# Performance work log

Hardware: AMD Instinct MI355X
Metric: run time of the kernel (lower is better)

Reference implementation:

```python
import jax, jax.numpy as jnp
import numpy as np

N_USERS, N_ITEMS, D, E = 60000, 40000, 64, 1600000
N = N_USERS + N_ITEMS


def setup_inputs() -> dict:
    key = jax.random.key(0)
    ks = jax.random.split(key, 7)
    user_embedding = jax.random.normal(ks[0], (N_USERS, D), dtype=jnp.float32)
    item_embedding = jax.random.normal(ks[1], (N_ITEMS, D), dtype=jnp.float32)
    # per-node symmetric-normalization scalar (e.g. 1/sqrt(deg)), positive
    norm = jax.random.uniform(ks[2], (N, 1), dtype=jnp.float32, minval=0.01, maxval=1.0)
    src = jax.random.randint(ks[3], (E,), 0, N, dtype=jnp.int32)
    dst = jax.random.randint(ks[4], (E,), 0, N, dtype=jnp.int32)
    # xavier-uniform linear weights, stored as [out_dim, in_dim] like nn.Linear
    limit = float(np.sqrt(6.0 / (D + D)))
    W1 = jax.random.uniform(ks[5], (D, D), dtype=jnp.float32, minval=-limit, maxval=limit)
    W2 = jax.random.uniform(ks[6], (D, D), dtype=jnp.float32, minval=-limit, maxval=limit)
    return {"user_embedding": user_embedding, "item_embedding": item_embedding,
            "norm": norm, "src": src, "dst": dst, "W1": W1, "W2": W2}


def reference(user_embedding, item_embedding, norm, src, dst, W1, W2):
    h = jnp.concatenate([user_embedding, item_embedding], axis=0)  # [N, D]
    # W1(h) can be computed once per node, then gathered per edge.
    h1 = h @ W1.T                                                  # [N, D]
    hs = h[src]                                                    # [E, D] gather
    hd = h[dst]                                                    # [E, D] gather
    # message: W1(h_src) + W2(h_src * h_dst), scaled by norm_src * norm_dst
    msg = (h1[src] + (hs * hd) @ W2.T) * (norm[src] * norm[dst])   # [E, D]
    m = jax.ops.segment_sum(msg, dst, num_segments=h.shape[0])     # scatter-sum -> [N, D]
    m = m + h1
    out = jnp.where(m >= 0, m, 0.2 * m)  # LeakyReLU(0.2); dropout=0 (eval) is identity
    # F.normalize(p=2, dim=1), eps=1e-12
    l2 = jnp.sqrt(jnp.sum(out * out, axis=1, keepdims=True))
    return out / jnp.maximum(l2, 1e-12)
```

## Files before the change

kernel.cpp:

```cpp
#include <hip/hip_runtime.h>

#define DD 64

typedef __attribute__((ext_vector_type(8))) short bfrag;
typedef __attribute__((ext_vector_type(4))) float ffrag;

static __device__ __forceinline__ short f2bf(float f) {
  union { float f; unsigned u; } v; v.f = f;
  unsigned r = v.u + 0x7fff + ((v.u >> 16) & 1);
  return (short)(r >> 16);
}
static __device__ __forceinline__ float bf2f(unsigned short u) {
  union { unsigned u; float f; } v; v.u = ((unsigned)u) << 16; return v.f;
}


__global__ void chist_kernel(const int* __restrict__ dst, int* __restrict__ ccnt,
                             int E, int NB) {
  __shared__ int ch[512];
  for (int i = threadIdx.x; i < 512; i += 256) ch[i] = 0;
  __syncthreads();
  int ebase = blockIdx.x * 4096;
#pragma unroll
  for (int j = 0; j < 16; ++j) {
    int e = ebase + j * 256 + threadIdx.x;
    if (e < E) atomicAdd(&ch[dst[e] >> 8], 1);
  }
  __syncthreads();
  for (int b = threadIdx.x; b < NB; b += 256) {
    int c = ch[b];
    if (c) atomicAdd(&ccnt[b], c);
  }
}

__global__ void cscan_kernel(const int* __restrict__ ccnt, int* __restrict__ cbase,
                             int* __restrict__ ccursor, int NB) {
  __shared__ int wtot[4];
  int t = threadIdx.x;
  int i0 = t * 2, i1 = t * 2 + 1;
  int v0 = (i0 < NB) ? ccnt[i0] : 0;
  int v1 = (i1 < NB) ? ccnt[i1] : 0;
  int s = v0 + v1;
  int lane = t & 63, w = t >> 6;
  int ps = s;
#pragma unroll
  for (int off = 1; off < 64; off <<= 1) {
    int tmp = __shfl_up(ps, off);
    if (lane >= off) ps += tmp;
  }
  if (lane == 63) wtot[w] = ps;
  __syncthreads();
  int wbase = 0;
  for (int k = 0; k < w; ++k) wbase += wtot[k];
  int excl = wbase + ps - s;
  if (i0 < NB) { cbase[i0] = excl;      ccursor[i0] = excl; }
  if (i1 < NB) { cbase[i1] = excl + v0; ccursor[i1] = excl + v0; }
  if (t == 0) {
    int tot = 0;
    for (int k = 0; k < 4; ++k) tot += wtot[k];
    cbase[NB] = tot;
  }
}

__global__ void cscatter_kernel(const int* __restrict__ src, const int* __restrict__ dst,
                                int* __restrict__ ccursor, unsigned* __restrict__ pairb,
                                int E, int NB) {
  __shared__ int bh[512], bbase[512], brank[512];
  for (int i = threadIdx.x; i < 512; i += 256) { bh[i] = 0; brank[i] = 0; }
  __syncthreads();
  int ebase = blockIdx.x * 4096;
  int se[16], de[16];
#pragma unroll
  for (int j = 0; j < 16; ++j) {
    int e = ebase + j * 256 + threadIdx.x;
    if (e < E) {
      se[j] = src[e];
      de[j] = dst[e];
      atomicAdd(&bh[de[j] >> 8], 1);
    } else {
      se[j] = -1; de[j] = 0;
    }
  }
  __syncthreads();
  for (int b = threadIdx.x; b < NB; b += 256) {
    int c = bh[b];
    bbase[b] = c ? atomicAdd(&ccursor[b], c) : 0;
  }
  __syncthreads();
#pragma unroll
  for (int j = 0; j < 16; ++j) {
    if (se[j] >= 0) {
      int b = de[j] >> 8;
      int r = atomicAdd(&brank[b], 1);
      pairb[bbase[b] + r] = ((unsigned)se[j] << 8) | (unsigned)(de[j] & 255);
    }
  }
}

__global__ void fine_kernel(const unsigned* __restrict__ pairb,
                            const int* __restrict__ cbase,
                            int* __restrict__ offs, int* __restrict__ cnt,
                            int* __restrict__ ebuf, int Nn) {
  __shared__ int fh[256], fcur[256];
  __shared__ int wtot[4];
  int t = threadIdx.x, b = blockIdx.x;
  int nb0 = b << 8;
  int cbeg = cbase[b], cend = cbase[b + 1];
  fh[t] = 0;
  __syncthreads();
  for (int p = cbeg + t; p < cend; p += 256) atomicAdd(&fh[pairb[p] & 255u], 1);
  __syncthreads();
  int val = fh[t];
  int lane = t & 63, w = t >> 6;
  int ps = val;
#pragma unroll
  for (int off = 1; off < 64; off <<= 1) {
    int tmp = __shfl_up(ps, off);
    if (lane >= off) ps += tmp;
  }
  if (lane == 63) wtot[w] = ps;
  __syncthreads();
  int wbase = 0;
  for (int k = 0; k < w; ++k) wbase += wtot[k];
  int excl = wbase + ps - val;
  int node = nb0 + t;
  if (node < Nn) { offs[node] = cbeg + excl; cnt[node] = val; }
  fcur[t] = cbeg + excl;
  __syncthreads();
  for (int p = cbeg + t; p < cend; p += 256) {
    unsigned v = pairb[p];
    int pos = atomicAdd(&fcur[v & 255u], 1);
    ebuf[pos] = (int)(v >> 8);
  }
}


__global__ void hconv_kernel(const float* __restrict__ ue, const float* __restrict__ ie,
                             const float* __restrict__ norm,
                             unsigned short* __restrict__ hsc, int Nn, int NU) {
  int tid = blockIdx.x * blockDim.x + threadIdx.x;
  if (tid >= Nn * 16) return;
  int row = tid >> 4;
  int q = tid & 15;
  const float* hr = (row < NU) ? ue + (size_t)row * DD : ie + (size_t)(row - NU) * DD;
  float nr = norm[row];
  float4 hv = reinterpret_cast<const float4*>(hr)[q];
  unsigned u0 = (unsigned short)f2bf(nr * hv.x);
  unsigned u1 = (unsigned short)f2bf(nr * hv.y);
  unsigned u2 = (unsigned short)f2bf(nr * hv.z);
  unsigned u3 = (unsigned short)f2bf(nr * hv.w);
  uint2 pk;
  pk.x = u0 | (u1 << 16);
  pk.y = u2 | (u3 << 16);
  *reinterpret_cast<uint2*>(hsc + (size_t)row * DD + q * 4) = pk;
}

__launch_bounds__(256)
__global__ void gather8_kernel(const unsigned short* __restrict__ hsc,
                               const int* __restrict__ offs,
                               const int* __restrict__ cnt,
                               const int* __restrict__ ebuf,
                               unsigned short* __restrict__ g, int Nn) {
  int lane = threadIdx.x & 63;
  int wid = blockIdx.x * 4 + (threadIdx.x >> 6);
  int d = __builtin_amdgcn_readfirstlane(wid);
  if (d >= Nn) return;
  int beg = __builtin_amdgcn_readfirstlane(offs[d]);
  int num = __builtin_amdgcn_readfirstlane(cnt[d]);
  float a0 = 0.f, a1 = 0.f, a2 = 0.f, a3 = 0.f;
  float a4 = 0.f, a5 = 0.f, a6 = 0.f, a7 = 0.f;
  int i = 0;
  for (; i + 8 <= num; i += 8) {
    int s0 = ebuf[beg + i + 0];
    int s1 = ebuf[beg + i + 1];
    int s2 = ebuf[beg + i + 2];
    int s3 = ebuf[beg + i + 3];
    int s4 = ebuf[beg + i + 4];
    int s5 = ebuf[beg + i + 5];
    int s6 = ebuf[beg + i + 6];
    int s7 = ebuf[beg + i + 7];
    a0 += bf2f(hsc[(size_t)s0 * DD + lane]);
    a1 += bf2f(hsc[(size_t)s1 * DD + lane]);
    a2 += bf2f(hsc[(size_t)s2 * DD + lane]);
    a3 += bf2f(hsc[(size_t)s3 * DD + lane]);
    a4 += bf2f(hsc[(size_t)s4 * DD + lane]);
    a5 += bf2f(hsc[(size_t)s5 * DD + lane]);
    a6 += bf2f(hsc[(size_t)s6 * DD + lane]);
    a7 += bf2f(hsc[(size_t)s7 * DD + lane]);
  }
  for (; i + 4 <= num; i += 4) {
    int s0 = ebuf[beg + i + 0];
    int s1 = ebuf[beg + i + 1];
    int s2 = ebuf[beg + i + 2];
    int s3 = ebuf[beg + i + 3];
    a0 += bf2f(hsc[(size_t)s0 * DD + lane]);
    a1 += bf2f(hsc[(size_t)s1 * DD + lane]);
    a2 += bf2f(hsc[(size_t)s2 * DD + lane]);
    a3 += bf2f(hsc[(size_t)s3 * DD + lane]);
  }
  for (; i < num; ++i) a0 += bf2f(hsc[(size_t)ebuf[beg + i] * DD + lane]);
  float r = ((a0 + a1) + (a2 + a3)) + ((a4 + a5) + (a6 + a7));
  g[(size_t)d * DD + lane] = (unsigned short)f2bf(r);
}

__launch_bounds__(256)
__global__ void gather8f_kernel(const unsigned short* __restrict__ hsc,
                                const int* __restrict__ offs,
                                const int* __restrict__ cnt,
                                const int* __restrict__ ebuf,
                                float* __restrict__ g, int Nn) {
  int lane = threadIdx.x & 63;
  int wid = blockIdx.x * 4 + (threadIdx.x >> 6);
  int d = __builtin_amdgcn_readfirstlane(wid);
  if (d >= Nn) return;
  int beg = __builtin_amdgcn_readfirstlane(offs[d]);
  int num = __builtin_amdgcn_readfirstlane(cnt[d]);
  float a0 = 0.f, a1 = 0.f, a2 = 0.f, a3 = 0.f;
  float a4 = 0.f, a5 = 0.f, a6 = 0.f, a7 = 0.f;
  int i = 0;
  for (; i + 8 <= num; i += 8) {
    int s0 = ebuf[beg + i + 0];
    int s1 = ebuf[beg + i + 1];
    int s2 = ebuf[beg + i + 2];
    int s3 = ebuf[beg + i + 3];
    int s4 = ebuf[beg + i + 4];
    int s5 = ebuf[beg + i + 5];
    int s6 = ebuf[beg + i + 6];
    int s7 = ebuf[beg + i + 7];
    a0 += bf2f(hsc[(size_t)s0 * DD + lane]);
    a1 += bf2f(hsc[(size_t)s1 * DD + lane]);
    a2 += bf2f(hsc[(size_t)s2 * DD + lane]);
    a3 += bf2f(hsc[(size_t)s3 * DD + lane]);
    a4 += bf2f(hsc[(size_t)s4 * DD + lane]);
    a5 += bf2f(hsc[(size_t)s5 * DD + lane]);
    a6 += bf2f(hsc[(size_t)s6 * DD + lane]);
    a7 += bf2f(hsc[(size_t)s7 * DD + lane]);
  }
  for (; i + 4 <= num; i += 4) {
    int s0 = ebuf[beg + i + 0];
    int s1 = ebuf[beg + i + 1];
    int s2 = ebuf[beg + i + 2];
    int s3 = ebuf[beg + i + 3];
    a0 += bf2f(hsc[(size_t)s0 * DD + lane]);
    a1 += bf2f(hsc[(size_t)s1 * DD + lane]);
    a2 += bf2f(hsc[(size_t)s2 * DD + lane]);
    a3 += bf2f(hsc[(size_t)s3 * DD + lane]);
  }
  for (; i < num; ++i) a0 += bf2f(hsc[(size_t)ebuf[beg + i] * DD + lane]);
  g[(size_t)d * DD + lane] = ((a0 + a1) + (a2 + a3)) + ((a4 + a5) + (a6 + a7));
}

__launch_bounds__(256)
__global__ void node_hsc_kernel(const unsigned short* __restrict__ hsc,
                                const unsigned short* __restrict__ g,
                                const float* __restrict__ norm,
                                const float* __restrict__ W1,
                                const float* __restrict__ W2,
                                float* __restrict__ out, int Nn) {
  int lane = threadIdx.x & 63;
  int l15 = lane & 15;
  int lg  = lane >> 4;
  int tile = blockIdx.x * 4 + (threadIdx.x >> 6);

  bfrag w1f[2][4], w2f[2][4];
#pragma unroll
  for (int jt = 0; jt < 4; ++jt) {
    int wrow = jt * 16 + l15;
#pragma unroll
    for (int ks = 0; ks < 2; ++ks) {
      int kb = ks * 32 + lg * 8;
      const float* p1 = W1 + wrow * DD + kb;
      const float* p2 = W2 + wrow * DD + kb;
#pragma unroll
      for (int j = 0; j < 8; ++j) {
        w1f[ks][jt][j] = f2bf(p1[j]);
        w2f[ks][jt][j] = f2bf(p2[j]);
      }
    }
  }

  if (tile * 16 >= Nn) return;
  int node = tile * 16 + l15;
  int nc = (node < Nn) ? node : (Nn - 1);
  float nd = norm[nc];
  float rnd = 1.0f / nd;

  ffrag acc[4];
#pragma unroll
  for (int jt = 0; jt < 4; ++jt) acc[jt] = (ffrag){0.f, 0.f, 0.f, 0.f};

#pragma unroll
  for (int ks = 0; ks < 2; ++ks) {
    int kb = ks * 32 + lg * 8;
    bfrag gb = *reinterpret_cast<const bfrag*>(g + (size_t)nc * DD + kb);
    bfrag hb = *reinterpret_cast<const bfrag*>(hsc + (size_t)nc * DD + kb);
    bfrag xf, yf;
#pragma unroll
    for (int j = 0; j < 8; ++j) {
      float gv = bf2f((unsigned short)gb[j]);
      float hj = bf2f((unsigned short)hb[j]);
      xf[j] = f2bf(fmaf(nd, gv, hj * rnd));
      yf[j] = f2bf(gv * hj);
    }
#pragma unroll
    for (int jt = 0; jt < 4; ++jt) {
      acc[jt] = __builtin_amdgcn_mfma_f32_16x16x32_bf16(xf, w1f[ks][jt], acc[jt], 0, 0, 0);
      acc[jt] = __builtin_amdgcn_mfma_f32_16x16x32_bf16(yf, w2f[ks][jt], acc[jt], 0, 0, 0);
    }
  }

  float v[4][4];
  float ss[4];
#pragma unroll
  for (int r = 0; r < 4; ++r) {
    float s = 0.f;
#pragma unroll
    for (int jt = 0; jt < 4; ++jt) {
      float m = acc[jt][r];
      float t = (m >= 0.f) ? m : 0.2f * m;
      v[r][jt] = t;
      s = fmaf(t, t, s);
    }
#pragma unroll
    for (int off = 1; off < 16; off <<= 1) s += __shfl_xor(s, off);
    ss[r] = s;
  }
#pragma unroll
  for (int r = 0; r < 4; ++r) {
    int orow = tile * 16 + lg * 4 + r;
    if (orow < Nn) {
      float inv = 1.0f / fmaxf(sqrtf(ss[r]), 1e-12f);
#pragma unroll
      for (int jt = 0; jt < 4; ++jt)
        out[(size_t)orow * DD + jt * 16 + l15] = v[r][jt] * inv;
    }
  }
}

__launch_bounds__(256)
__global__ void node_hscf_kernel(const unsigned short* __restrict__ hsc,
                                 const float* __restrict__ g,
                                 const float* __restrict__ norm,
                                 const float* __restrict__ W1,
                                 const float* __restrict__ W2,
                                 float* __restrict__ out, int Nn) {
  int lane = threadIdx.x & 63;
  int l15 = lane & 15;
  int lg  = lane >> 4;
  int tile = blockIdx.x * 4 + (threadIdx.x >> 6);

  bfrag w1f[2][4], w2f[2][4];
#pragma unroll
  for (int jt = 0; jt < 4; ++jt) {
    int wrow = jt * 16 + l15;
#pragma unroll
    for (int ks = 0; ks < 2; ++ks) {
      int kb = ks * 32 + lg * 8;
      const float* p1 = W1 + wrow * DD + kb;
      const float* p2 = W2 + wrow * DD + kb;
#pragma unroll
      for (int j = 0; j < 8; ++j) {
        w1f[ks][jt][j] = f2bf(p1[j]);
        w2f[ks][jt][j] = f2bf(p2[j]);
      }
    }
  }

  if (tile * 16 >= Nn) return;
  int node = tile * 16 + l15;
  int nc = (node < Nn) ? node : (Nn - 1);
  float nd = norm[nc];
  float rnd = 1.0f / nd;

  ffrag acc[4];
#pragma unroll
  for (int jt = 0; jt < 4; ++jt) acc[jt] = (ffrag){0.f, 0.f, 0.f, 0.f};

#pragma unroll
  for (int ks = 0; ks < 2; ++ks) {
    int kb = ks * 32 + lg * 8;
    float4 g0 = *reinterpret_cast<const float4*>(g + (size_t)nc * DD + kb);
    float4 g1 = *reinterpret_cast<const float4*>(g + (size_t)nc * DD + kb + 4);
    bfrag hb = *reinterpret_cast<const bfrag*>(hsc + (size_t)nc * DD + kb);
    float gv[8] = {g0.x, g0.y, g0.z, g0.w, g1.x, g1.y, g1.z, g1.w};
    bfrag xf, yf;
#pragma unroll
    for (int j = 0; j < 8; ++j) {
      float hj = bf2f((unsigned short)hb[j]);
      xf[j] = f2bf(fmaf(nd, gv[j], hj * rnd));
      yf[j] = f2bf(gv[j] * hj);
    }
#pragma unroll
    for (int jt = 0; jt < 4; ++jt) {
      acc[jt] = __builtin_amdgcn_mfma_f32_16x16x32_bf16(xf, w1f[ks][jt], acc[jt], 0, 0, 0);
      acc[jt] = __builtin_amdgcn_mfma_f32_16x16x32_bf16(yf, w2f[ks][jt], acc[jt], 0, 0, 0);
    }
  }

  float v[4][4];
  float ss[4];
#pragma unroll
  for (int r = 0; r < 4; ++r) {
    float s = 0.f;
#pragma unroll
    for (int jt = 0; jt < 4; ++jt) {
      float m = acc[jt][r];
      float t = (m >= 0.f) ? m : 0.2f * m;
      v[r][jt] = t;
      s = fmaf(t, t, s);
    }
#pragma unroll
    for (int off = 1; off < 16; off <<= 1) s += __shfl_xor(s, off);
    ss[r] = s;
  }
#pragma unroll
  for (int r = 0; r < 4; ++r) {
    int orow = tile * 16 + lg * 4 + r;
    if (orow < Nn) {
      float inv = 1.0f / fmaxf(sqrtf(ss[r]), 1e-12f);
#pragma unroll
      for (int jt = 0; jt < 4; ++jt)
        out[(size_t)orow * DD + jt * 16 + l15] = v[r][jt] * inv;
    }
  }
}


extern "C" void kernel_launch(void* const* d_in, const int* in_sizes, int n_in,
                              void* d_out, int out_size, void* d_ws, size_t ws_size,
                              hipStream_t stream) {
  const float* ue   = (const float*)d_in[0];
  const float* ie   = (const float*)d_in[1];
  const float* norm = (const float*)d_in[2];
  const int*   src  = (const int*)d_in[3];
  const int*   dst  = (const int*)d_in[4];
  const float* W1   = (const float*)d_in[5];
  const float* W2   = (const float*)d_in[6];
  float* out = (float*)d_out;

  int NU = in_sizes[0] / DD;
  int Nn = in_sizes[2];
  int E  = in_sizes[3];

  int NB = (Nn + 255) >> 8;
  if (NB > 512) return;

  size_t un      = ((size_t)E > (size_t)Nn * 32) ? (size_t)E : (size_t)Nn * 32;
  size_t base_ints = 1538 + 2 * (size_t)Nn + (size_t)E + un + 16;
  size_t g_ints    = (size_t)Nn * 32;
  size_t ext_ints  = base_ints + g_ints + 16;

  int* ccnt    = (int*)d_ws;
  int* cbase   = ccnt + 512;
  int* ccursor = cbase + 513;
  int* offs    = ccnt + 1538;
  int* cnt     = offs + Nn;
  int* ebuf    = cnt + Nn;
  uintptr_t up = (uintptr_t)(ebuf + E);
  up = (up + 15) & ~(uintptr_t)15;
  unsigned*       pairb = (unsigned*)up;
  unsigned short* hsc   = (unsigned short*)up;

  hipMemsetAsync(ccnt, 0, 512 * sizeof(int), stream);

  int EB = (E + 4095) / 4096;
  chist_kernel<<<EB, 256, 0, stream>>>(dst, ccnt, E, NB);
  cscan_kernel<<<1, 256, 0, stream>>>(ccnt, cbase, ccursor, NB);
  cscatter_kernel<<<EB, 256, 0, stream>>>(src, dst, ccursor, pairb, E, NB);
  fine_kernel<<<NB, 256, 0, stream>>>(pairb, cbase, offs, cnt, ebuf, Nn);
  hconv_kernel<<<(Nn * 16 + 255) / 256, 256, 0, stream>>>(ue, ie, norm, hsc, Nn, NU);

  int gblk = (Nn + 3) / 4;
  int ntiles = (Nn + 15) / 16;
  int nblk = (ntiles + 3) / 4;

  if (ws_size >= ext_ints * sizeof(int)) {
    uintptr_t gp = up + un * sizeof(int);
    gp = (gp + 15) & ~(uintptr_t)15;
    unsigned short* gbuf = (unsigned short*)gp;
    gather8_kernel<<<gblk, 256, 0, stream>>>(hsc, offs, cnt, ebuf, gbuf, Nn);
    node_hsc_kernel<<<nblk, 256, 0, stream>>>(hsc, gbuf, norm, W1, W2, out, Nn);
  } else {
    gather8f_kernel<<<gblk, 256, 0, stream>>>(hsc, offs, cnt, ebuf, out, Nn);
    node_hscf_kernel<<<nblk, 256, 0, stream>>>(hsc, out, norm, W1, W2, out, Nn);
  }
}
```

Baseline: 149.9 us.

## Fuse edge sort and bf16 conversion into one cooperative grid-synced kernel

Result: slower. 535.7 us (+257.3%).

```diff
diff --git a/kernel.cpp b/kernel.cpp
--- a/kernel.cpp
+++ b/kernel.cpp
@@ -1,4 +1,7 @@
 #include <hip/hip_runtime.h>
+#include <hip/hip_cooperative_groups.h>
+
+namespace cg = cooperative_groups;
 
 #define DD 64
 
@@ -12,6 +15,166 @@
 }
 static __device__ __forceinline__ float bf2f(unsigned short u) {
   union { unsigned u; float f; } v; v.u = ((unsigned)u) << 16; return v.f;
+}
+
+
+__launch_bounds__(256)
+__global__ void sort_hconv_coop(const int* __restrict__ src, const int* __restrict__ dst,
+                                const float* __restrict__ ue, const float* __restrict__ ie,
+                                const float* __restrict__ norm,
+                                int* __restrict__ ccnt, int* __restrict__ cbase,
+                                int* __restrict__ ccursor,
+                                int* __restrict__ offs, int* __restrict__ cnt,
+                                int* __restrict__ ebuf, unsigned* __restrict__ pairb,
+                                unsigned short* __restrict__ hsc,
+                                int E, int NB, int Nn, int NU) {
+  cg::grid_group grid = cg::this_grid();
+  int t = threadIdx.x;
+  int b = blockIdx.x;
+  int nblk = gridDim.x;
+
+  __shared__ int ch[512];
+  __shared__ int bh[512], bbase[512], brank[512];
+  __shared__ int fh[256], fcur[256];
+  __shared__ int wtot[4];
+
+  if (b == 0) {
+    for (int i = t; i < 512; i += 256) ccnt[i] = 0;
+  }
+  __threadfence();
+  grid.sync();
+
+  {
+    for (int i = t; i < 512; i += 256) ch[i] = 0;
+    __syncthreads();
+    int ebase = b * 4096;
+#pragma unroll
+    for (int j = 0; j < 16; ++j) {
+      int e = ebase + j * 256 + t;
+      if (e < E) atomicAdd(&ch[dst[e] >> 8], 1);
+    }
+    __syncthreads();
+    for (int i = t; i < NB; i += 256) {
+      int c = ch[i];
+      if (c) atomicAdd(&ccnt[i], c);
+    }
+  }
+  __threadfence();
+  grid.sync();
+
+  if (b == 0) {
+    int i0 = t * 2, i1 = t * 2 + 1;
+    int v0 = (i0 < NB) ? ccnt[i0] : 0;
+    int v1 = (i1 < NB) ? ccnt[i1] : 0;
+    int s = v0 + v1;
+    int lane = t & 63, w = t >> 6;
+    int ps = s;
+#pragma unroll
+    for (int off = 1; off < 64; off <<= 1) {
+      int tmp = __shfl_up(ps, off);
+      if (lane >= off) ps += tmp;
+    }
+    if (lane == 63) wtot[w] = ps;
+    __syncthreads();
+    int wbase = 0;
+    for (int k = 0; k < w; ++k) wbase += wtot[k];
+    int excl = wbase + ps - s;
+    if (i0 < NB) { cbase[i0] = excl;      ccursor[i0] = excl; }
+    if (i1 < NB) { cbase[i1] = excl + v0; ccursor[i1] = excl + v0; }
+    if (t == 0) {
+      int tot = 0;
+      for (int k = 0; k < 4; ++k) tot += wtot[k];
+      cbase[NB] = tot;
+    }
+  }
+  __threadfence();
+  grid.sync();
+
+  {
+    for (int i = t; i < 512; i += 256) { bh[i] = 0; brank[i] = 0; }
+    __syncthreads();
+    int ebase = b * 4096;
+    int se[16], de[16];
+#pragma unroll
+    for (int j = 0; j < 16; ++j) {
+      int e = ebase + j * 256 + t;
+      if (e < E) {
+        se[j] = src[e];
+        de[j] = dst[e];
+        atomicAdd(&bh[de[j] >> 8], 1);
+      } else {
+        se[j] = -1; de[j] = 0;
+      }
+    }
+    __syncthreads();
+    for (int i = t; i < NB; i += 256) {
+      int c = bh[i];
+      bbase[i] = c ? atomicAdd(&ccursor[i], c) : 0;
+    }
+    __syncthreads();
+#pragma unroll
+    for (int j = 0; j < 16; ++j) {
+      if (se[j] >= 0) {
+        int bb = de[j] >> 8;
+        int r = atomicAdd(&brank[bb], 1);
+        pairb[bbase[bb] + r] = ((unsigned)se[j] << 8) | (unsigned)(de[j] & 255);
+      }
+    }
+  }
+  __threadfence();
+  grid.sync();
+
+  if (b < NB) {
+    int nb0 = b << 8;
+    int cbeg = cbase[b], cend = cbase[b + 1];
+    fh[t] = 0;
+    __syncthreads();
+    for (int p = cbeg + t; p < cend; p += 256) atomicAdd(&fh[pairb[p] & 255u], 1);
+    __syncthreads();
+    int val = fh[t];
+    int lane = t & 63, w = t >> 6;
+    int ps = val;
+#pragma unroll
+    for (int off = 1; off < 64; off <<= 1) {
+      int tmp = __shfl_up(ps, off);
+      if (lane >= off) ps += tmp;
+    }
+    if (lane == 63) wtot[w] = ps;
+    __syncthreads();
+    int wbase = 0;
+    for (int k = 0; k < w; ++k) wbase += wtot[k];
+    int excl = wbase + ps - val;
+    int node = nb0 + t;
+    if (node < Nn) { offs[node] = cbeg + excl; cnt[node] = val; }
+    fcur[t] = cbeg + excl;
+    __syncthreads();
+    for (int p = cbeg + t; p < cend; p += 256) {
+      unsigned v = pairb[p];
+      int pos = atomicAdd(&fcur[v & 255u], 1);
+      ebuf[pos] = (int)(v >> 8);
+    }
+  }
+  __threadfence();
+  grid.sync();
+
+  {
+    int total = Nn * 16;
+    for (int idx = b * 256 + t; idx < total; idx += nblk * 256) {
+      int row = idx >> 4;
+      int q = idx & 15;
+      const float* hr = (row < NU) ? ue + (size_t)row * DD : ie + (size_t)(row - NU) * DD;
+      float nr = norm[row];
+      float4 hv = reinterpret_cast<const float4*>(hr)[q];
+      unsigned u0 = (unsigned short)f2bf(nr * hv.x);
+      unsigned u1 = (unsigned short)f2bf(nr * hv.y);
+      unsigned u2 = (unsigned short)f2bf(nr * hv.z);
+      unsigned u3 = (unsigned short)f2bf(nr * hv.w);
+      uint2 pk;
+      pk.x = u0 | (u1 << 16);
+      pk.y = u2 | (u3 << 16);
+      *reinterpret_cast<uint2*>(hsc + (size_t)row * DD + q * 4) = pk;
+    }
+  }
 }
 
 
@@ -133,7 +296,6 @@
     ebuf[pos] = (int)(v >> 8);
   }
 }
-
 
 __global__ void hconv_kernel(const float* __restrict__ ue, const float* __restrict__ ie,
                              const float* __restrict__ norm,
@@ -444,8 +606,9 @@
 
   int NB = (Nn + 255) >> 8;
   if (NB > 512) return;
-
-  size_t un      = ((size_t)E > (size_t)Nn * 32) ? (size_t)E : (size_t)Nn * 32;
+  int EB = (E + 4095) / 4096;
+
+  size_t un        = ((size_t)E > (size_t)Nn * 32) ? (size_t)E : (size_t)Nn * 32;
   size_t base_ints = 1538 + 2 * (size_t)Nn + (size_t)E + un + 16;
   size_t g_ints    = (size_t)Nn * 32;
   size_t ext_ints  = base_ints + g_ints + 16;
@@ -461,14 +624,24 @@
   unsigned*       pairb = (unsigned*)up;
   unsigned short* hsc   = (unsigned short*)up;
 
-  hipMemsetAsync(ccnt, 0, 512 * sizeof(int), stream);
-
-  int EB = (E + 4095) / 4096;
-  chist_kernel<<<EB, 256, 0, stream>>>(dst, ccnt, E, NB);
-  cscan_kernel<<<1, 256, 0, stream>>>(ccnt, cbase, ccursor, NB);
-  cscatter_kernel<<<EB, 256, 0, stream>>>(src, dst, ccursor, pairb, E, NB);
-  fine_kernel<<<NB, 256, 0, stream>>>(pairb, cbase, offs, cnt, ebuf, Nn);
-  hconv_kernel<<<(Nn * 16 + 255) / 256, 256, 0, stream>>>(ue, ie, norm, hsc, Nn, NU);
+  int grid = (EB > NB) ? EB : NB;
+  bool use_coop = (grid <= 1024);
+
+  if (use_coop) {
+    void* kargs[] = {(void*)&src, (void*)&dst, (void*)&ue, (void*)&ie, (void*)&norm,
+                     (void*)&ccnt, (void*)&cbase, (void*)&ccursor, (void*)&offs,
+                     (void*)&cnt, (void*)&ebuf, (void*)&pairb, (void*)&hsc,
+                     (void*)&E, (void*)&NB, (void*)&Nn, (void*)&NU};
+    hipLaunchCooperativeKernel((void*)sort_hconv_coop, dim3(grid), dim3(256),
+                               kargs, 0, stream);
+  } else {
+    hipMemsetAsync(ccnt, 0, 512 * sizeof(int), stream);
+    chist_kernel<<<EB, 256, 0, stream>>>(dst, ccnt, E, NB);
+    cscan_kernel<<<1, 256, 0, stream>>>(ccnt, cbase, ccursor, NB);
+    cscatter_kernel<<<EB, 256, 0, stream>>>(src, dst, ccursor, pairb, E, NB);
+    fine_kernel<<<NB, 256, 0, stream>>>(pairb, cbase, offs, cnt, ebuf, Nn);
+    hconv_kernel<<<(Nn * 16 + 255) / 256, 256, 0, stream>>>(ue, ie, norm, hsc, Nn, NU);
+  }
 
   int gblk = (Nn + 3) / 4;
   int ntiles = (Nn + 15) / 16;
```

## Replace histogram-and-scan CSR build with fixed-capacity bucket scatter

Applied to the files above, without the earlier changes.

Result: faster. 136.6 us (-8.9%).

```diff
diff --git a/kernel.cpp b/kernel.cpp
--- a/kernel.cpp
+++ b/kernel.cpp
@@ -1,6 +1,7 @@
 #include <hip/hip_runtime.h>
 
 #define DD 64
+#define CAPB 8192
 
 typedef __attribute__((ext_vector_type(8))) short bfrag;
 typedef __attribute__((ext_vector_type(4))) float ffrag;
@@ -14,57 +15,16 @@
   union { unsigned u; float f; } v; v.u = ((unsigned)u) << 16; return v.f;
 }
 
-
-__global__ void chist_kernel(const int* __restrict__ dst, int* __restrict__ ccnt,
-                             int E, int NB) {
-  __shared__ int ch[512];
-  for (int i = threadIdx.x; i < 512; i += 256) ch[i] = 0;
-  __syncthreads();
-  int ebase = blockIdx.x * 4096;
-#pragma unroll
-  for (int j = 0; j < 16; ++j) {
-    int e = ebase + j * 256 + threadIdx.x;
-    if (e < E) atomicAdd(&ch[dst[e] >> 8], 1);
-  }
-  __syncthreads();
-  for (int b = threadIdx.x; b < NB; b += 256) {
-    int c = ch[b];
-    if (c) atomicAdd(&ccnt[b], c);
-  }
-}
-
-__global__ void cscan_kernel(const int* __restrict__ ccnt, int* __restrict__ cbase,
-                             int* __restrict__ ccursor, int NB) {
-  __shared__ int wtot[4];
+__global__ void init_kernel(int* __restrict__ ctrl) {
   int t = threadIdx.x;
-  int i0 = t * 2, i1 = t * 2 + 1;
-  int v0 = (i0 < NB) ? ccnt[i0] : 0;
-  int v1 = (i1 < NB) ? ccnt[i1] : 0;
-  int s = v0 + v1;
-  int lane = t & 63, w = t >> 6;
-  int ps = s;
-#pragma unroll
-  for (int off = 1; off < 64; off <<= 1) {
-    int tmp = __shfl_up(ps, off);
-    if (lane >= off) ps += tmp;
-  }
-  if (lane == 63) wtot[w] = ps;
-  __syncthreads();
-  int wbase = 0;
-  for (int k = 0; k < w; ++k) wbase += wtot[k];
-  int excl = wbase + ps - s;
-  if (i0 < NB) { cbase[i0] = excl;      ccursor[i0] = excl; }
-  if (i1 < NB) { cbase[i1] = excl + v0; ccursor[i1] = excl + v0; }
-  if (t == 0) {
-    int tot = 0;
-    for (int k = 0; k < 4; ++k) tot += wtot[k];
-    cbase[NB] = tot;
-  }
-}
-
-__global__ void cscatter_kernel(const int* __restrict__ src, const int* __restrict__ dst,
-                                int* __restrict__ ccursor, unsigned* __restrict__ pairb,
-                                int E, int NB) {
+  for (int i = t; i < 512; i += 256) ctrl[i] = i * CAPB;
+  if (t == 0) ctrl[512] = 0;
+}
+
+__global__ void cscatter_bump_kernel(const int* __restrict__ src,
+                                     const int* __restrict__ dst,
+                                     int* __restrict__ ccursor,
+                                     unsigned* __restrict__ pairb, int E, int NB) {
   __shared__ int bh[512], bbase[512], brank[512];
   for (int i = threadIdx.x; i < 512; i += 256) { bh[i] = 0; brank[i] = 0; }
   __syncthreads();
@@ -90,22 +50,27 @@
 #pragma unroll
   for (int j = 0; j < 16; ++j) {
     if (se[j] >= 0) {
-      int b = de[j] >> 8;
-      int r = atomicAdd(&brank[b], 1);
-      pairb[bbase[b] + r] = ((unsigned)se[j] << 8) | (unsigned)(de[j] & 255);
-    }
-  }
-}
-
-__global__ void fine_kernel(const unsigned* __restrict__ pairb,
-                            const int* __restrict__ cbase,
-                            int* __restrict__ offs, int* __restrict__ cnt,
-                            int* __restrict__ ebuf, int Nn) {
+      int bb = de[j] >> 8;
+      int r = atomicAdd(&brank[bb], 1);
+      int pos = bbase[bb] + r;
+      if (pos < (bb + 1) * CAPB)
+        pairb[pos] = ((unsigned)se[j] << 8) | (unsigned)(de[j] & 255);
+    }
+  }
+}
+
+__global__ void fine2_kernel(const unsigned* __restrict__ pairb,
+                             const int* __restrict__ ccursor, int* __restrict__ gcount,
+                             int* __restrict__ offs, int* __restrict__ cnt,
+                             int* __restrict__ ebuf, int Nn) {
   __shared__ int fh[256], fcur[256];
   __shared__ int wtot[4];
+  __shared__ int ebase_sh;
   int t = threadIdx.x, b = blockIdx.x;
   int nb0 = b << 8;
-  int cbeg = cbase[b], cend = cbase[b + 1];
+  int cbeg = b * CAPB;
+  int cend = ccursor[b];
+  int total = cend - cbeg;
   fh[t] = 0;
   __syncthreads();
   for (int p = cbeg + t; p < cend; p += 256) atomicAdd(&fh[pairb[p] & 255u], 1);
@@ -119,13 +84,15 @@
     if (lane >= off) ps += tmp;
   }
   if (lane == 63) wtot[w] = ps;
+  if (t == 0) ebase_sh = atomicAdd(gcount, total);
   __syncthreads();
   int wbase = 0;
   for (int k = 0; k < w; ++k) wbase += wtot[k];
   int excl = wbase + ps - val;
+  int ebase = ebase_sh;
   int node = nb0 + t;
-  if (node < Nn) { offs[node] = cbeg + excl; cnt[node] = val; }
-  fcur[t] = cbeg + excl;
+  if (node < Nn) { offs[node] = ebase + excl; cnt[node] = val; }
+  fcur[t] = ebase + excl;
   __syncthreads();
   for (int p = cbeg + t; p < cend; p += 256) {
     unsigned v = pairb[p];
@@ -133,7 +100,6 @@
     ebuf[pos] = (int)(v >> 8);
   }
 }
-
 
 __global__ void hconv_kernel(const float* __restrict__ ue, const float* __restrict__ ie,
                              const float* __restrict__ norm,
@@ -444,16 +410,20 @@
 
   int NB = (Nn + 255) >> 8;
   if (NB > 512) return;
-
-  size_t un      = ((size_t)E > (size_t)Nn * 32) ? (size_t)E : (size_t)Nn * 32;
+  int EB = (E + 4095) / 4096;
+
+  size_t unA = (size_t)NB * CAPB;
+  size_t unB = (size_t)Nn * 32;
+  size_t un  = (unA > unB) ? unA : unB;
+  if ((size_t)E > un) un = (size_t)E;
   size_t base_ints = 1538 + 2 * (size_t)Nn + (size_t)E + un + 16;
   size_t g_ints    = (size_t)Nn * 32;
   size_t ext_ints  = base_ints + g_ints + 16;
 
-  int* ccnt    = (int*)d_ws;
-  int* cbase   = ccnt + 512;
-  int* ccursor = cbase + 513;
-  int* offs    = ccnt + 1538;
+  int* ctrl    = (int*)d_ws;
+  int* ccursor = ctrl;
+  int* gcount  = ctrl + 512;
+  int* offs    = ctrl + 1538;
   int* cnt     = offs + Nn;
   int* ebuf    = cnt + Nn;
   uintptr_t up = (uintptr_t)(ebuf + E);
@@ -461,13 +431,9 @@
   unsigned*       pairb = (unsigned*)up;
   unsigned short* hsc   = (unsigned short*)up;
 
-  hipMemsetAsync(ccnt, 0, 512 * sizeof(int), stream);
-
-  int EB = (E + 4095) / 4096;
-  chist_kernel<<<EB, 256, 0, stream>>>(dst, ccnt, E, NB);
-  cscan_kernel<<<1, 256, 0, stream>>>(ccnt, cbase, ccursor, NB);
-  cscatter_kernel<<<EB, 256, 0, stream>>>(src, dst, ccursor, pairb, E, NB);
-  fine_kernel<<<NB, 256, 0, stream>>>(pairb, cbase, offs, cnt, ebuf, Nn);
+  init_kernel<<<1, 256, 0, stream>>>(ctrl);
+  cscatter_bump_kernel<<<EB, 256, 0, stream>>>(src, dst, ccursor, pairb, E, NB);
+  fine2_kernel<<<NB, 256, 0, stream>>>(pairb, ccursor, gcount, offs, cnt, ebuf, Nn);
   hconv_kernel<<<(Nn * 16 + 255) / 256, 256, 0, stream>>>(ue, ie, norm, hsc, Nn, NU);
 
   int gblk = (Nn + 3) / 4;
```
